# Performance work log

Hardware: AMD Instinct MI355X
Metric: run time of the kernel (lower is better)

## Reference

```python
import jax, jax.numpy as jnp
import numpy as np

BASE = 10000.0

def _rope_neox(x, positions, head_dim):
    # x: [B, S, n_heads, head_dim]; positions: [B, S] int
    half = head_dim // 2
    inv_freq = 1.0 / (BASE ** (jnp.arange(0, head_dim, 2, dtype=jnp.float32) / head_dim))  # [half]
    freqs = positions.astype(jnp.float32)[..., None] * inv_freq  # [B, S, half]
    cos = jnp.cos(freqs)[:, :, None, :]  # [B, S, 1, half]
    sin = jnp.sin(freqs)[:, :, None, :]
    x1, x2 = x[..., :half], x[..., half:]
    return jnp.concatenate([x1 * cos - x2 * sin, x2 * cos + x1 * sin], axis=-1)

def setup_inputs() -> dict:
    key = jax.random.key(0)
    k1, k2, k3 = jax.random.split(key, 3)
    B, S, H = 1, 2048, 4096
    hidden_states = jax.random.normal(k1, (B, S, H), dtype=jnp.float32)
    position_ids = jnp.broadcast_to(jnp.arange(S, dtype=jnp.int32), (B, S))
    W_qkv = jax.random.normal(k2, (H, 3 * H), dtype=jnp.float32) * (H ** -0.5)
    W_o = jax.random.normal(k3, (H, H), dtype=jnp.float32) * (H ** -0.5)
    return {"hidden_states": hidden_states, "position_ids": position_ids, "W_qkv": W_qkv, "W_o": W_o}

def reference(hidden_states, position_ids, W_qkv, W_o):
    B, S, H = hidden_states.shape
    n_heads = 32
    head_dim = H // n_heads
    qkv = hidden_states @ W_qkv  # [B, S, 3H]
    q, k, v = jnp.split(qkv, 3, axis=-1)
    q = q.reshape(B, S, n_heads, head_dim)
    k = k.reshape(B, S, n_heads, head_dim)
    v = v.reshape(B, S, n_heads, head_dim)
    q = _rope_neox(q, position_ids, head_dim)
    k = _rope_neox(k, position_ids, head_dim)
    # causal SDPA (past_key_value=None -> is_causal=True)
    scale = 1.0 / jnp.sqrt(jnp.float32(head_dim))
    scores = jnp.einsum('bqhd,bkhd->bhqk', q, k) * scale  # [B, nH, S, S]
    causal = jnp.tril(jnp.ones((S, S), dtype=bool))
    scores = jnp.where(causal, scores, jnp.finfo(scores.dtype).min)
    probs = jax.nn.softmax(scores, axis=-1)
    attn = jnp.einsum('bhqk,bkhd->bqhd', probs, v).reshape(B, S, H)
    return attn @ W_o
```

## Files before the change

kernel.cpp:

```cpp
#include <hip/hip_runtime.h>
#include <hip/hip_bf16.h>
#include <math.h>

#define SEQ   2048
#define HID   4096
#define NHEAD 32
#define HD    128
#define QKVN  12288

typedef __bf16 bf16;
typedef __bf16 bf16x8 __attribute__((ext_vector_type(8)));
typedef __bf16 bf16x4 __attribute__((ext_vector_type(4)));
typedef float  f32x4  __attribute__((ext_vector_type(4)));

#define AS1 __attribute__((address_space(1)))
#define AS3 __attribute__((address_space(3)))

__device__ __forceinline__ void gload16(const void* g, void* l) {
    __builtin_amdgcn_global_load_lds((const AS1 void*)g, (AS3 void*)l, 16, 0, 0);
}

__device__ __forceinline__ unsigned short bbits(bf16 b) {
    union { bf16 b; unsigned short u; } x; x.b = b; return x.u;
}

__global__ __launch_bounds__(512) __attribute__((amdgpu_waves_per_eu(2, 2)))
void gemm256(const bf16* __restrict__ A, const bf16* __restrict__ Bt,
             bf16* __restrict__ C, int M, int N, int K, int bcol0) {
    __shared__ __attribute__((aligned(16))) char lds[131072];
    const int tid  = threadIdx.x;
    const int l    = tid & 63;
    const int wave = tid >> 6;
    const int wr   = wave >> 2;
    const int wc   = wave & 3;
    const int lh   = l >> 4;
    const int ll   = l & 15;
    const int by   = blockIdx.x & 7, bx = blockIdx.x >> 3;
    const int brow = by * 256, bcol = bcol0 + bx * 256;

    f32x4 acc[4][4][2];
    #pragma unroll
    for (int q = 0; q < 4; ++q)
        #pragma unroll
        for (int f = 0; f < 4; ++f)
            #pragma unroll
            for (int g = 0; g < 2; ++g) acc[q][f][g] = (f32x4){0.f, 0.f, 0.f, 0.f};

    const int trow = tid >> 3, tslot = tid & 7;
    const int srcs = (tslot ^ (trow & 7)) * 16;
    const size_t rowb = (size_t)K * 2;
    const char* pA[2][2]; const char* pB[2][2];
    #pragma unroll
    for (int h = 0; h < 2; ++h)
        #pragma unroll
        for (int i = 0; i < 2; ++i) {
            pA[h][i] = (const char*)A  + (size_t)(brow + h*128 + i*64 + trow) * rowb + srcs;
            pB[h][i] = (const char*)Bt + (size_t)(bcol + h*128 + i*64 + trow) * rowb + srcs;
        }

#define SA(buf, h) do { \
        gload16(pA[h][0], lds + (buf)*65536 + (h)*16384 + tid*16); \
        gload16(pA[h][1], lds + (buf)*65536 + (h)*16384 + 8192 + tid*16); \
        pA[h][0] += 128; pA[h][1] += 128; \
    } while (0)
#define SB(buf, h) do { \
        gload16(pB[h][0], lds + (buf)*65536 + 32768 + (h)*16384 + tid*16); \
        gload16(pB[h][1], lds + (buf)*65536 + 32768 + (h)*16384 + 8192 + tid*16); \
        pB[h][0] += 128; pB[h][1] += 128; \
    } while (0)

    const int sw0 = ((0 + lh) ^ (ll & 7)) << 4;
    const int sw1 = ((4 + lh) ^ (ll & 7)) << 4;

    bf16x8 af[4][2], bv0[2][2], bv1[2][2];

#define LOADA(Xb, mh) do { \
        const char* LA_ = lds + (Xb)*65536 + (mh)*16384 + (wr*64 + ll)*128; \
        _Pragma("unroll") \
        for (int f_ = 0; f_ < 4; ++f_) { \
            af[f_][0] = *(const bf16x8*)(LA_ + f_*2048 + sw0); \
            af[f_][1] = *(const bf16x8*)(LA_ + f_*2048 + sw1); \
        } \
    } while (0)
#define LOADB(Xb, nh, bvv) do { \
        const char* LB_ = lds + (Xb)*65536 + 32768 + (nh)*16384 + (wc*32 + ll)*128; \
        _Pragma("unroll") \
        for (int g_ = 0; g_ < 2; ++g_) { \
            bvv[g_][0] = *(const bf16x8*)(LB_ + g_*2048 + sw0); \
            bvv[g_][1] = *(const bf16x8*)(LB_ + g_*2048 + sw1); \
        } \
    } while (0)
#define FENCE_MMA(WAITSTR, q, bvv) do { \
        asm volatile(WAITSTR ::: "memory"); \
        __builtin_amdgcn_s_barrier(); \
        asm volatile("s_waitcnt lgkmcnt(0)" ::: "memory"); \
        __builtin_amdgcn_sched_barrier(0); \
        __builtin_amdgcn_s_setprio(1); \
        _Pragma("unroll") \
        for (int f_ = 0; f_ < 4; ++f_) \
            _Pragma("unroll") \
            for (int g_ = 0; g_ < 2; ++g_) { \
                acc[q][f_][g_] = __builtin_amdgcn_mfma_f32_16x16x32_bf16( \
                    af[f_][0], bvv[g_][0], acc[q][f_][g_], 0, 0, 0); \
                acc[q][f_][g_] = __builtin_amdgcn_mfma_f32_16x16x32_bf16( \
                    af[f_][1], bvv[g_][1], acc[q][f_][g_], 0, 0, 0); \
            } \
        __builtin_amdgcn_s_setprio(0); \
        __builtin_amdgcn_s_barrier(); \
    } while (0)

    SA(0, 0); SB(0, 0); SB(0, 1); SA(0, 1); SA(1, 0); SB(1, 0);
    asm volatile("s_waitcnt vmcnt(8)" ::: "memory");
    __builtin_amdgcn_s_barrier();

    const int NT = K >> 6;
    for (int u = 0; u < NT - 1; ++u) {
        const int X = u & 1, Y = X ^ 1;
        LOADA(X, 0); LOADB(X, 0, bv0); SB(Y, 1);
        FENCE_MMA("s_waitcnt vmcnt(8)", 0, bv0);
        LOADB(X, 1, bv1); SA(Y, 1);
        FENCE_MMA("s_waitcnt vmcnt(8)", 1, bv1);
        LOADA(X, 1);
        if (u < NT - 2) { SA(X, 0); }
        FENCE_MMA("s_waitcnt vmcnt(8)", 2, bv0);
        if (u < NT - 2) { SB(X, 0); }
        FENCE_MMA("s_waitcnt vmcnt(8)", 3, bv1);
    }
    {
        const int X = (NT - 1) & 1;
        LOADA(X, 0); LOADB(X, 0, bv0);
        FENCE_MMA("s_waitcnt vmcnt(4)", 0, bv0);
        LOADB(X, 1, bv1);
        FENCE_MMA("s_waitcnt vmcnt(2)", 1, bv1);
        LOADA(X, 1);
        FENCE_MMA("s_waitcnt vmcnt(0)", 2, bv0);
        FENCE_MMA("s_nop 0", 3, bv1);
    }
#undef FENCE_MMA
#undef LOADA
#undef LOADB
#undef SA
#undef SB

    __syncthreads();
    float* ep = (float*)lds + wave * 2304;
    const int c8 = (l & 3) * 8;
    #pragma unroll
    for (int q = 0; q < 4; ++q) {
        const int mh = q >> 1, nh = q & 1;
        #pragma unroll
        for (int f = 0; f < 4; ++f)
            #pragma unroll
            for (int g = 0; g < 2; ++g)
                #pragma unroll
                for (int j = 0; j < 4; ++j)
                    ep[(f*16 + lh*4 + j) * 36 + g*16 + ll] = acc[q][f][g][j];
        #pragma unroll
        for (int it = 0; it < 4; ++it) {
            int r2 = it * 16 + (l >> 2);
            const float* src = ep + r2 * 36 + c8;
            bf16x8 o;
            #pragma unroll
            for (int j = 0; j < 8; ++j) o[j] = (bf16)src[j];
            size_t grow = (size_t)(brow + mh*128 + wr*64 + r2);
            *(bf16x8*)(C + grow * N + bcol + nh*128 + wc*32 + c8) = o;
        }
    }
}

template<int OB>
__global__ __launch_bounds__(512, 2) void gemm2p(const bf16* __restrict__ A,
                                                 const bf16* __restrict__ Bt,
                                                 void* __restrict__ Cv,
                                                 int M, int N, int K, int bcol0) {
    __shared__ __attribute__((aligned(16))) char lds[98304];
    const int tid  = threadIdx.x;
    const int l    = tid & 63;
    const int wave = tid >> 6;
    const int wr   = wave >> 2;
    const int wc   = wave & 3;
    const int lh   = l >> 4;
    const int ll   = l & 15;

    const int by   = blockIdx.x & 7;
    const int bx   = blockIdx.x >> 3;
    const int brow = by * 256, bcol = bcol0 + bx * 128;

    f32x4 acc[2][4][2];
    #pragma unroll
    for (int m = 0; m < 2; ++m)
        #pragma unroll
        for (int f = 0; f < 4; ++f)
            #pragma unroll
            for (int g = 0; g < 2; ++g) acc[m][f][g] = (f32x4){0.f, 0.f, 0.f, 0.f};

    const int trow = tid >> 3, tslot = tid & 7;
    const int srcs = (tslot ^ (trow & 7)) * 16;
    const size_t rowb = (size_t)K * 2;
    const char* pA[2][2]; const char* pB[2];
    #pragma unroll
    for (int h = 0; h < 2; ++h)
        #pragma unroll
        for (int i = 0; i < 2; ++i)
            pA[h][i] = (const char*)A + (size_t)(brow + h*128 + i*64 + trow) * rowb + srcs;
    #pragma unroll
    for (int i = 0; i < 2; ++i)
        pB[i] = (const char*)Bt + (size_t)(bcol + i*64 + trow) * rowb + srcs;

#define SA(buf, h) do { \
        gload16(pA[h][0], lds + (buf)*32768 + (h)*16384 + tid*16); \
        gload16(pA[h][1], lds + (buf)*32768 + (h)*16384 + 8192 + tid*16); \
        pA[h][0] += 128; pA[h][1] += 128; \
    } while (0)
#define SB(buf) do { \
        gload16(pB[0], lds + 65536 + (buf)*16384 + tid*16); \
        gload16(pB[1], lds + 65536 + (buf)*16384 + 8192 + tid*16); \
        pB[0] += 128; pB[1] += 128; \
    } while (0)

    const int sw0 = ((0 + lh) ^ (ll & 7)) << 4;
    const int sw1 = ((4 + lh) ^ (ll & 7)) << 4;

#define PHASE(Xb, mh, STAGE_STMT, WAITSTR) do { \
        const char* LA_ = lds + (Xb)*32768 + (mh)*16384 + (wr*64 + ll)*128; \
        const char* LB_ = lds + 65536 + (Xb)*16384 + (wc*32 + ll)*128; \
        bf16x8 af_[4][2], bv_[2][2]; \
        _Pragma("unroll") \
        for (int f_ = 0; f_ < 4; ++f_) { \
            af_[f_][0] = *(const bf16x8*)(LA_ + f_*2048 + sw0); \
            af_[f_][1] = *(const bf16x8*)(LA_ + f_*2048 + sw1); \
        } \
        _Pragma("unroll") \
        for (int g_ = 0; g_ < 2; ++g_) { \
            bv_[g_][0] = *(const bf16x8*)(LB_ + g_*2048 + sw0); \
            bv_[g_][1] = *(const bf16x8*)(LB_ + g_*2048 + sw1); \
        } \
        STAGE_STMT; \
        asm volatile(WAITSTR ::: "memory"); \
        __builtin_amdgcn_s_barrier(); \
        asm volatile("s_waitcnt lgkmcnt(0)" ::: "memory"); \
        __builtin_amdgcn_sched_barrier(0); \
        __builtin_amdgcn_s_setprio(1); \
        _Pragma("unroll") \
        for (int f_ = 0; f_ < 4; ++f_) \
            _Pragma("unroll") \
            for (int g_ = 0; g_ < 2; ++g_) { \
                acc[mh][f_][g_] = __builtin_amdgcn_mfma_f32_16x16x32_bf16( \
                    af_[f_][0], bv_[g_][0], acc[mh][f_][g_], 0, 0, 0); \
                acc[mh][f_][g_] = __builtin_amdgcn_mfma_f32_16x16x32_bf16( \
                    af_[f_][1], bv_[g_][1], acc[mh][f_][g_], 0, 0, 0); \
            } \
        __builtin_amdgcn_s_setprio(0); \
        __builtin_amdgcn_s_barrier(); \
    } while (0)

    SA(0, 0); SB(0); SA(0, 1); SA(1, 0);
    asm volatile("s_waitcnt vmcnt(4)" ::: "memory");
    __builtin_amdgcn_s_barrier();

    const int NT = K >> 6;
    for (int u = 0; u < NT - 2; ++u) {
        const int X = u & 1, Y = X ^ 1;
        PHASE(X, 0, SB(Y), "s_waitcnt vmcnt(4)");
        PHASE(X, 1, { SA(Y, 1); SA(X, 0); }, "s_waitcnt vmcnt(4)");
    }
    {
        const int X = (NT - 2) & 1, Y = X ^ 1;
        PHASE(X, 0, SB(Y), "s_waitcnt vmcnt(4)");
        PHASE(X, 1, SA(Y, 1), "s_waitcnt vmcnt(2)");
    }
    {
        const int X = (NT - 1) & 1;
        PHASE(X, 0, ((void)0), "s_waitcnt vmcnt(0)");
        PHASE(X, 1, ((void)0), "s_nop 0");
    }
#undef PHASE
#undef SA
#undef SB

    __syncthreads();
    float* ep = (float*)lds + wave * 2304;
    const int cq = l & 3;
    #pragma unroll
    for (int mh = 0; mh < 2; ++mh) {
        #pragma unroll
        for (int f = 0; f < 4; ++f)
            #pragma unroll
            for (int g = 0; g < 2; ++g)
                #pragma unroll
                for (int j = 0; j < 4; ++j)
                    ep[(f*16 + lh*4 + j) * 36 + g*16 + ll] = acc[mh][f][g][j];
        #pragma unroll
        for (int it = 0; it < 4; ++it) {
            int r2 = it * 16 + (l >> 2);
            const float* src = ep + r2 * 36 + cq * 8;
            size_t grow = (size_t)(brow + mh*128 + wr*64 + r2);
            int gcol = bcol + wc*32 + cq*8;
            if (OB == 0) {
                float* dst = (float*)Cv + grow * N + gcol;
                *(f32x4*)dst       = *(const f32x4*)src;
                *(f32x4*)(dst + 4) = *(const f32x4*)(src + 4);
            } else {
                bf16x8 o;
                #pragma unroll
                for (int jj = 0; jj < 8; ++jj) o[jj] = (bf16)src[jj];
                *(bf16x8*)((bf16*)Cv + grow * N + gcol) = o;
            }
        }
    }
}

__global__ __launch_bounds__(256) void cast_flat(const float* __restrict__ in,
                                                 bf16* __restrict__ out, int n8) {
    int i = blockIdx.x * 256 + threadIdx.x;
    if (i >= n8) return;
    float4 a = ((const float4*)in)[2 * i];
    float4 b = ((const float4*)in)[2 * i + 1];
    bf16x8 o = {(bf16)a.x, (bf16)a.y, (bf16)a.z, (bf16)a.w,
                (bf16)b.x, (bf16)b.y, (bf16)b.z, (bf16)b.w};
    *(bf16x8*)(out + (size_t)i * 8) = o;
}

__global__ __launch_bounds__(256) void cast_transpose(const float* __restrict__ in,
                                                      bf16* __restrict__ out, int R, int C) {
    __shared__ float t[64][65];
    const int r0 = blockIdx.y * 64, c0 = blockIdx.x * 64;
    #pragma unroll
    for (int i = 0; i < 4; ++i) {
        int idx = i * 256 + threadIdx.x;
        int rr = idx >> 4, c4 = (idx & 15) * 4;
        float4 v = *(const float4*)&in[(size_t)(r0 + rr) * C + c0 + c4];
        t[rr][c4] = v.x; t[rr][c4 + 1] = v.y; t[rr][c4 + 2] = v.z; t[rr][c4 + 3] = v.w;
    }
    __syncthreads();
    #pragma unroll
    for (int i = 0; i < 2; ++i) {
        int idx = i * 256 + threadIdx.x;
        int rr = idx >> 3, c8 = (idx & 7) * 8;
        bf16x8 o;
        #pragma unroll
        for (int j = 0; j < 8; ++j) o[j] = (bf16)t[c8 + j][rr];
        *(bf16x8*)&out[(size_t)(c0 + rr) * R + r0 + c8] = o;
    }
}

__global__ __launch_bounds__(256) void rope_table(const int* __restrict__ pos_ids,
                                                  float2* __restrict__ tab) {
    int id = blockIdx.x * 256 + threadIdx.x;
    int s = id >> 6, d = id & 63;
    float pos = (float)pos_ids[s];
    float inv = expf(-9.210340371976184f * ((float)d * (1.0f / 64.0f)));
    float sn, cs;
    sincosf(pos * inv, &sn, &cs);
    tab[id] = make_float2(cs, sn);
}

__global__ __launch_bounds__(256) void rope_repack(const bf16* __restrict__ qkv,
                                                   const float2* __restrict__ tab,
                                                   bf16* __restrict__ Qb,
                                                   bf16* __restrict__ Kb) {
    int id = blockIdx.x * 256 + threadIdx.x;
    const int d4 = (id & 15) * 4;
    const int h  = (id >> 4) & (NHEAD - 1);
    const int s  = id >> 9;

    float2 tr[4];
    #pragma unroll
    for (int i = 0; i < 4; ++i) tr[i] = tab[s * 64 + d4 + i];

    const bf16* row = qkv + (size_t)s * QKVN;
    {
        bf16x4 lo = *(const bf16x4*)(row + h * HD + d4);
        bf16x4 hi = *(const bf16x4*)(row + h * HD + 64 + d4);
        bf16x4 olo, ohi;
        #pragma unroll
        for (int i = 0; i < 4; ++i) {
            float x1 = (float)lo[i], x2 = (float)hi[i];
            olo[i] = (bf16)(x1 * tr[i].x - x2 * tr[i].y);
            ohi[i] = (bf16)(x2 * tr[i].x + x1 * tr[i].y);
        }
        bf16* qo = Qb + ((size_t)h * SEQ + s) * HD;
        *(bf16x4*)(qo + d4) = olo;
        *(bf16x4*)(qo + 64 + d4) = ohi;
    }
    {
        bf16x4 lo = *(const bf16x4*)(row + HID + h * HD + d4);
        bf16x4 hi = *(const bf16x4*)(row + HID + h * HD + 64 + d4);
        bf16x4 olo, ohi;
        #pragma unroll
        for (int i = 0; i < 4; ++i) {
            float x1 = (float)lo[i], x2 = (float)hi[i];
            olo[i] = (bf16)(x1 * tr[i].x - x2 * tr[i].y);
            ohi[i] = (bf16)(x2 * tr[i].x + x1 * tr[i].y);
        }
        bf16* ko = Kb + ((size_t)h * SEQ + s) * HD;
        *(bf16x4*)(ko + d4) = olo;
        *(bf16x4*)(ko + 64 + d4) = ohi;
    }
}

__global__ __launch_bounds__(256) void v_transpose(const bf16* __restrict__ qkv,
                                                   bf16* __restrict__ Vt) {
    __shared__ bf16 t[64][130];
    const int h = blockIdx.y, s0 = blockIdx.x * 64;
    #pragma unroll
    for (int i = 0; i < 4; ++i) {
        int idx = i * 256 + threadIdx.x;
        int ss = idx >> 4, c8 = (idx & 15) * 8;
        bf16x8 v = *(const bf16x8*)&qkv[(size_t)(s0 + ss) * QKVN + 2 * HID + h * HD + c8];
        #pragma unroll
        for (int j = 0; j < 8; ++j) t[ss][c8 + j] = v[j];
    }
    __syncthreads();
    #pragma unroll
    for (int i = 0; i < 4; ++i) {
        int idx = i * 256 + threadIdx.x;
        int dd = idx >> 3, s8 = (idx & 7) * 8;
        bf16x8 o;
        #pragma unroll
        for (int j = 0; j < 8; ++j) o[j] = t[s8 + j][dd];
        *(bf16x8*)&Vt[((size_t)h * HD + dd) * SEQ + s0 + s8] = o;
    }
}

__global__ __launch_bounds__(256) void attn_mfma(const bf16* __restrict__ Qb,
                                                 const bf16* __restrict__ Kb,
                                                 const bf16* __restrict__ Vt,
                                                 bf16* __restrict__ attn) {
    __shared__ __attribute__((aligned(16))) char Ka[2][16384];
    __shared__ __attribute__((aligned(16))) char Va[2][16384];
    __shared__ __attribute__((aligned(16))) char Ps[4 * 2048];
    const int tid  = threadIdx.x, l = tid & 63, wave = tid >> 6;
    const int head = blockIdx.x;
    const int qb   = gridDim.y - 1 - blockIdx.y;
    const int q0   = qb * 64;
    const int qw   = q0 + wave * 16;
    const float scale = 0.08838834764831845f;

    bf16x8 qf[4];
    const bf16* Qg = Qb + ((size_t)head * SEQ + qw + (l & 15)) * HD;
    #pragma unroll
    for (int kc = 0; kc < 4; ++kc) qf[kc] = *(const bf16x8*)(Qg + kc * 32 + (l >> 4) * 8);

    f32x4 o[8];
    #pragma unroll
    for (int i = 0; i < 8; ++i) o[i] = (f32x4){0.f, 0.f, 0.f, 0.f};
    float mrun = -1e30f, lrun = 0.f;
    const int qrow  = qw + (l & 15);
    const int ntile = qb + 1;

    const char* Kg = (const char*)(Kb + (size_t)head * SEQ * HD);
    const char* Vg = (const char*)(Vt + (size_t)head * HD * SEQ);
    char* Pw = Ps + wave * 2048;

#define ASTAGE(b, t0) do { \
        const int kv0_ = (t0) * 64; \
        _Pragma("unroll") \
        for (int i = 0; i < 4; ++i) { \
            int c = i * 256 + tid; \
            int rk_ = c >> 4, slk_ = c & 15; \
            gload16(Kg + (size_t)(kv0_ + rk_) * 256 + ((slk_ * 16) ^ ((rk_ & 15) << 4)), \
                    Ka[b] + (size_t)(i * 256 + (tid & 192)) * 16); \
            int rv_ = c >> 3, slv_ = c & 7; \
            gload16(Vg + (size_t)rv_ * (SEQ * 2) + (size_t)kv0_ * 2 + ((slv_ * 16) ^ ((rv_ & 7) << 4)), \
                    Va[b] + (size_t)(i * 256 + (tid & 192)) * 16); \
        } \
    } while (0)

    ASTAGE(0, 0);
    asm volatile("s_waitcnt vmcnt(0)" ::: "memory");
    __builtin_amdgcn_s_barrier();

    for (int t = 0; t < ntile; ++t) {
        const int cur = t & 1;
        const int kv0 = t * 64;
        if (t + 1 < ntile) ASTAGE(cur ^ 1, t + 1);

        f32x4 st[4];
        __builtin_amdgcn_s_setprio(1);
        #pragma unroll
        for (int mf = 0; mf < 4; ++mf) {
            f32x4 s = (f32x4){0.f, 0.f, 0.f, 0.f};
            #pragma unroll
            for (int kc = 0; kc < 4; ++kc) {
                int rk = mf * 16 + (l & 15);
                bf16x8 a = *(const bf16x8*)(Ka[cur] + rk * 256 +
                              ((kc * 64 + (l >> 4) * 16) ^ ((rk & 15) << 4)));
                s = __builtin_amdgcn_mfma_f32_16x16x32_bf16(a, qf[kc], s, 0, 0, 0);
            }
            st[mf] = s;
        }
        __builtin_amdgcn_s_setprio(0);

        float pm = -1e30f;
        #pragma unroll
        for (int mf = 0; mf < 4; ++mf)
            #pragma unroll
            for (int j = 0; j < 4; ++j) {
                int kv = kv0 + mf * 16 + (l >> 4) * 4 + j;
                float v = (kv <= qrow) ? st[mf][j] * scale : -1e30f;
                st[mf][j] = v;
                pm = fmaxf(pm, v);
            }
        pm = fmaxf(pm, __shfl_xor(pm, 16));
        pm = fmaxf(pm, __shfl_xor(pm, 32));
        float mn   = fmaxf(mrun, pm);
        float corr = __expf(mrun - mn);
        float ls = 0.f;
        #pragma unroll
        for (int mf = 0; mf < 4; ++mf)
            #pragma unroll
            for (int j = 0; j < 4; ++j) {
                float p = __expf(st[mf][j] - mn);
                st[mf][j] = p;
                ls += p;
            }
        ls += __shfl_xor(ls, 16);
        ls += __shfl_xor(ls, 32);
        lrun = lrun * corr + ls;
        mrun = mn;

        f32x4 cv;
        #pragma unroll
        for (int r = 0; r < 4; ++r) cv[r] = __shfl(corr, (l >> 4) * 4 + r, 64);
        #pragma unroll
        for (int nf = 0; nf < 8; ++nf) o[nf] *= cv;

        #pragma unroll
        for (int mf = 0; mf < 4; ++mf)
            #pragma unroll
            for (int r = 0; r < 4; r += 2) {
                int kv = mf * 16 + (l >> 4) * 4 + r;
                unsigned pk = (unsigned)bbits((bf16)st[mf][r]) |
                              ((unsigned)bbits((bf16)st[mf][r + 1]) << 16);
                *(unsigned*)(Pw + (l & 15) * 128 + ((kv * 2) ^ ((l & 15 & 7) << 4))) = pk;
            }

        __builtin_amdgcn_s_setprio(1);
        #pragma unroll
        for (int kc = 0; kc < 2; ++kc) {
            bf16x8 pa = *(const bf16x8*)(Pw + (l & 15) * 128 +
                           ((kc * 64 + (l >> 4) * 16) ^ ((l & 7) << 4)));
            #pragma unroll
            for (int nf = 0; nf < 8; ++nf) {
                int dr = nf * 16 + (l & 15);
                bf16x8 vb = *(const bf16x8*)(Va[cur] + dr * 128 +
                               ((kc * 64 + (l >> 4) * 16) ^ ((dr & 7) << 4)));
                o[nf] = __builtin_amdgcn_mfma_f32_16x16x32_bf16(pa, vb, o[nf], 0, 0, 0);
            }
        }
        __builtin_amdgcn_s_setprio(0);

        asm volatile("s_waitcnt vmcnt(0) lgkmcnt(0)" ::: "memory");
        __builtin_amdgcn_s_barrier();
    }
#undef ASTAGE

    float il = 1.0f / lrun;
    f32x4 iv;
    #pragma unroll
    for (int r = 0; r < 4; ++r) iv[r] = __shfl(il, (l >> 4) * 4 + r, 64);
    #pragma unroll
    for (int nf = 0; nf < 8; ++nf)
        #pragma unroll
        for (int r = 0; r < 4; ++r) {
            int row = qw + (l >> 4) * 4 + r;
            attn[(size_t)row * HID + head * HD + nf * 16 + (l & 15)] = (bf16)(o[nf][r] * iv[r]);
        }
}

extern "C" void kernel_launch(void* const* d_in, const int* in_sizes, int n_in,
                              void* d_out, int out_size, void* d_ws, size_t ws_size,
                              hipStream_t stream) {
    const float* hidden  = (const float*)d_in[0];
    const int*   pos_ids = (const int*)d_in[1];
    const float* W_qkv   = (const float*)d_in[2];
    const float* W_o     = (const float*)d_in[3];
    float*       out     = (float*)d_out;
    char*        ws      = (char*)d_ws;

    bf16*   Wqkv_t   = (bf16*)(ws);
    bf16*   qkv_b    = (bf16*)(ws + 100663296);
    bf16*   hidden_b = (bf16*)(ws + 150994944);
    float2* tab      = (float2*)(ws + 150994944);
    bf16* Qb     = (bf16*)(ws);
    bf16* Kb     = (bf16*)(ws + 16777216);
    bf16* Vtb    = (bf16*)(ws + 33554432);
    bf16* attn_b = (bf16*)(ws + 50331648);
    bf16* Wo_t   = (bf16*)(ws + 67108864);

    cast_flat<<<SEQ * HID / 8 / 256, 256, 0, stream>>>(hidden, hidden_b, SEQ * HID / 8);
    cast_transpose<<<dim3(QKVN / 64, HID / 64), 256, 0, stream>>>(W_qkv, Wqkv_t, HID, QKVN);
    gemm256<<<(8192 / 256) * (SEQ / 256), 512, 0, stream>>>(hidden_b, Wqkv_t, qkv_b,
                                                            SEQ, QKVN, HID, 0);
    gemm2p<1><<<(4096 / 128) * (SEQ / 256), 512, 0, stream>>>(hidden_b, Wqkv_t, qkv_b,
                                                              SEQ, QKVN, HID, 8192);
    rope_table<<<SEQ * 64 / 256, 256, 0, stream>>>(pos_ids, tab);
    rope_repack<<<SEQ * NHEAD * 16 / 256, 256, 0, stream>>>(qkv_b, tab, Qb, Kb);
    v_transpose<<<dim3(SEQ / 64, NHEAD), 256, 0, stream>>>(qkv_b, Vtb);
    cast_transpose<<<dim3(HID / 64, HID / 64), 256, 0, stream>>>(W_o, Wo_t, HID, HID);
    attn_mfma<<<dim3(NHEAD, SEQ / 64), 256, 0, stream>>>(Qb, Kb, Vtb, attn_b);
    gemm2p<0><<<(HID / 128) * (SEQ / 256), 512, 0, stream>>>(attn_b, Wo_t, out,
                                                             SEQ, HID, HID, 0);
}
```

Measured before the change: 438.3 us.

## Transpose GEMM tile to 128x256 with A fragments held across N halves

Replaces the 256x128 two-phase GEMM with a 128x256 tile variant. A fragments are loaded once per K-step and reused across two N-half phases, while B is staged in larger 32KB buffers. The block index mapping and the epilogue change to match, with a wider per-wave stride for the LDS staging of outputs. This targets LDS read traffic and global load balance in the V-projection and output GEMMs, but it changes the vmcnt pipelining and register pressure under a fixed two-waves-per-EU attribute.

```diff
diff --git a/kernel.cpp b/kernel.cpp
--- a/kernel.cpp
+++ b/kernel.cpp
@@ -169,10 +169,9 @@
 }
 
 template<int OB>
-__global__ __launch_bounds__(512, 2) void gemm2p(const bf16* __restrict__ A,
-                                                 const bf16* __restrict__ Bt,
-                                                 void* __restrict__ Cv,
-                                                 int M, int N, int K, int bcol0) {
+__global__ __launch_bounds__(512) __attribute__((amdgpu_waves_per_eu(2, 2)))
+void gemm128n(const bf16* __restrict__ A, const bf16* __restrict__ Bt,
+              void* __restrict__ Cv, int M, int N, int K, int bcol0) {
     __shared__ __attribute__((aligned(16))) char lds[98304];
     const int tid  = threadIdx.x;
     const int l    = tid & 63;
@@ -181,55 +180,55 @@
     const int wc   = wave & 3;
     const int lh   = l >> 4;
     const int ll   = l & 15;
-
-    const int by   = blockIdx.x & 7;
-    const int bx   = blockIdx.x >> 3;
-    const int brow = by * 256, bcol = bcol0 + bx * 128;
-
-    f32x4 acc[2][4][2];
-    #pragma unroll
-    for (int m = 0; m < 2; ++m)
-        #pragma unroll
-        for (int f = 0; f < 4; ++f)
-            #pragma unroll
-            for (int g = 0; g < 2; ++g) acc[m][f][g] = (f32x4){0.f, 0.f, 0.f, 0.f};
+    const int brow = (blockIdx.x & 15) * 128;
+    const int bcol = bcol0 + (blockIdx.x >> 4) * 256;
+
+    f32x4 acc[4][4];
+    #pragma unroll
+    for (int f = 0; f < 4; ++f)
+        #pragma unroll
+        for (int c = 0; c < 4; ++c) acc[f][c] = (f32x4){0.f, 0.f, 0.f, 0.f};
 
     const int trow = tid >> 3, tslot = tid & 7;
     const int srcs = (tslot ^ (trow & 7)) * 16;
     const size_t rowb = (size_t)K * 2;
-    const char* pA[2][2]; const char* pB[2];
-    #pragma unroll
-    for (int h = 0; h < 2; ++h)
-        #pragma unroll
-        for (int i = 0; i < 2; ++i)
-            pA[h][i] = (const char*)A + (size_t)(brow + h*128 + i*64 + trow) * rowb + srcs;
+    const char* pA[2]; const char* pB[4];
     #pragma unroll
     for (int i = 0; i < 2; ++i)
+        pA[i] = (const char*)A + (size_t)(brow + i*64 + trow) * rowb + srcs;
+    #pragma unroll
+    for (int i = 0; i < 4; ++i)
         pB[i] = (const char*)Bt + (size_t)(bcol + i*64 + trow) * rowb + srcs;
 
-#define SA(buf, h) do { \
-        gload16(pA[h][0], lds + (buf)*32768 + (h)*16384 + tid*16); \
-        gload16(pA[h][1], lds + (buf)*32768 + (h)*16384 + 8192 + tid*16); \
-        pA[h][0] += 128; pA[h][1] += 128; \
+#define SA(buf) do { \
+        gload16(pA[0], lds + (buf)*16384 + tid*16); \
+        gload16(pA[1], lds + (buf)*16384 + 8192 + tid*16); \
+        pA[0] += 128; pA[1] += 128; \
     } while (0)
 #define SB(buf) do { \
-        gload16(pB[0], lds + 65536 + (buf)*16384 + tid*16); \
-        gload16(pB[1], lds + 65536 + (buf)*16384 + 8192 + tid*16); \
-        pB[0] += 128; pB[1] += 128; \
+        gload16(pB[0], lds + 32768 + (buf)*32768 + tid*16); \
+        gload16(pB[1], lds + 32768 + (buf)*32768 + 8192 + tid*16); \
+        gload16(pB[2], lds + 32768 + (buf)*32768 + 16384 + tid*16); \
+        gload16(pB[3], lds + 32768 + (buf)*32768 + 24576 + tid*16); \
+        pB[0] += 128; pB[1] += 128; pB[2] += 128; pB[3] += 128; \
     } while (0)
 
     const int sw0 = ((0 + lh) ^ (ll & 7)) << 4;
     const int sw1 = ((4 + lh) ^ (ll & 7)) << 4;
 
-#define PHASE(Xb, mh, STAGE_STMT, WAITSTR) do { \
-        const char* LA_ = lds + (Xb)*32768 + (mh)*16384 + (wr*64 + ll)*128; \
-        const char* LB_ = lds + 65536 + (Xb)*16384 + (wc*32 + ll)*128; \
-        bf16x8 af_[4][2], bv_[2][2]; \
+    bf16x8 af[4][2];
+
+#define LOADA(Xb) do { \
+        const char* LA_ = lds + (Xb)*16384 + (wr*64 + ll)*128; \
         _Pragma("unroll") \
         for (int f_ = 0; f_ < 4; ++f_) { \
-            af_[f_][0] = *(const bf16x8*)(LA_ + f_*2048 + sw0); \
-            af_[f_][1] = *(const bf16x8*)(LA_ + f_*2048 + sw1); \
+            af[f_][0] = *(const bf16x8*)(LA_ + f_*2048 + sw0); \
+            af[f_][1] = *(const bf16x8*)(LA_ + f_*2048 + sw1); \
         } \
+    } while (0)
+#define PHASE(Xb, nh, STAGE_STMT, WAITSTR) do { \
+        const char* LB_ = lds + 32768 + (Xb)*32768 + (wc*64 + (nh)*32 + ll)*128; \
+        bf16x8 bv_[2][2]; \
         _Pragma("unroll") \
         for (int g_ = 0; g_ < 2; ++g_) { \
             bv_[g_][0] = *(const bf16x8*)(LB_ + g_*2048 + sw0); \
@@ -245,66 +244,71 @@
         for (int f_ = 0; f_ < 4; ++f_) \
             _Pragma("unroll") \
             for (int g_ = 0; g_ < 2; ++g_) { \
-                acc[mh][f_][g_] = __builtin_amdgcn_mfma_f32_16x16x32_bf16( \
-                    af_[f_][0], bv_[g_][0], acc[mh][f_][g_], 0, 0, 0); \
-                acc[mh][f_][g_] = __builtin_amdgcn_mfma_f32_16x16x32_bf16( \
-                    af_[f_][1], bv_[g_][1], acc[mh][f_][g_], 0, 0, 0); \
+                acc[f_][(nh)*2+g_] = __builtin_amdgcn_mfma_f32_16x16x32_bf16( \
+                    af[f_][0], bv_[g_][0], acc[f_][(nh)*2+g_], 0, 0, 0); \
+                acc[f_][(nh)*2+g_] = __builtin_amdgcn_mfma_f32_16x16x32_bf16( \
+                    af[f_][1], bv_[g_][1], acc[f_][(nh)*2+g_], 0, 0, 0); \
             } \
         __builtin_amdgcn_s_setprio(0); \
         __builtin_amdgcn_s_barrier(); \
     } while (0)
 
-    SA(0, 0); SB(0); SA(0, 1); SA(1, 0);
-    asm volatile("s_waitcnt vmcnt(4)" ::: "memory");
+    SA(0); SB(0); SA(1);
+    asm volatile("s_waitcnt vmcnt(2)" ::: "memory");
     __builtin_amdgcn_s_barrier();
 
     const int NT = K >> 6;
     for (int u = 0; u < NT - 2; ++u) {
         const int X = u & 1, Y = X ^ 1;
-        PHASE(X, 0, SB(Y), "s_waitcnt vmcnt(4)");
-        PHASE(X, 1, { SA(Y, 1); SA(X, 0); }, "s_waitcnt vmcnt(4)");
+        LOADA(X);
+        PHASE(X, 0, SB(Y), "s_waitcnt vmcnt(6)");
+        PHASE(X, 1, SA(X), "s_waitcnt vmcnt(6)");
     }
     {
         const int X = (NT - 2) & 1, Y = X ^ 1;
-        PHASE(X, 0, SB(Y), "s_waitcnt vmcnt(4)");
-        PHASE(X, 1, SA(Y, 1), "s_waitcnt vmcnt(2)");
+        LOADA(X);
+        PHASE(X, 0, SB(Y), "s_waitcnt vmcnt(6)");
+        PHASE(X, 1, ((void)0), "s_waitcnt vmcnt(4)");
     }
     {
         const int X = (NT - 1) & 1;
+        LOADA(X);
         PHASE(X, 0, ((void)0), "s_waitcnt vmcnt(0)");
         PHASE(X, 1, ((void)0), "s_nop 0");
     }
 #undef PHASE
+#undef LOADA
 #undef SA
 #undef SB
 
     __syncthreads();
-    float* ep = (float*)lds + wave * 2304;
-    const int cq = l & 3;
-    #pragma unroll
-    for (int mh = 0; mh < 2; ++mh) {
-        #pragma unroll
-        for (int f = 0; f < 4; ++f)
-            #pragma unroll
-            for (int g = 0; g < 2; ++g)
-                #pragma unroll
-                for (int j = 0; j < 4; ++j)
-                    ep[(f*16 + lh*4 + j) * 36 + g*16 + ll] = acc[mh][f][g][j];
-        #pragma unroll
-        for (int it = 0; it < 4; ++it) {
-            int r2 = it * 16 + (l >> 2);
-            const float* src = ep + r2 * 36 + cq * 8;
-            size_t grow = (size_t)(brow + mh*128 + wr*64 + r2);
-            int gcol = bcol + wc*32 + cq*8;
-            if (OB == 0) {
-                float* dst = (float*)Cv + grow * N + gcol;
-                *(f32x4*)dst       = *(const f32x4*)src;
-                *(f32x4*)(dst + 4) = *(const f32x4*)(src + 4);
-            } else {
+    float* ep = (float*)lds + wave * (16 * 68);
+    #pragma unroll
+    for (int f = 0; f < 4; ++f) {
+        #pragma unroll
+        for (int c = 0; c < 4; ++c)
+            #pragma unroll
+            for (int j = 0; j < 4; ++j)
+                ep[(lh*4 + j) * 68 + c*16 + ll] = acc[f][c][j];
+        if (OB == 0) {
+            #pragma unroll
+            for (int it = 0; it < 4; ++it) {
+                int row = it * 4 + (l >> 4);
+                const float* src = ep + row * 68 + (l & 15) * 4;
+                size_t grow = (size_t)(brow + wr*64 + f*16 + row);
+                *(f32x4*)((float*)Cv + grow * N + bcol + wc*64 + (l & 15) * 4) =
+                    *(const f32x4*)src;
+            }
+        } else {
+            #pragma unroll
+            for (int it = 0; it < 2; ++it) {
+                int row = it * 8 + (l >> 3);
+                const float* src = ep + row * 68 + (l & 7) * 8;
                 bf16x8 o;
                 #pragma unroll
-                for (int jj = 0; jj < 8; ++jj) o[jj] = (bf16)src[jj];
-                *(bf16x8*)((bf16*)Cv + grow * N + gcol) = o;
+                for (int j = 0; j < 8; ++j) o[j] = (bf16)src[j];
+                size_t grow = (size_t)(brow + wr*64 + f*16 + row);
+                *(bf16x8*)((bf16*)Cv + grow * N + bcol + wc*64 + (l & 7) * 8) = o;
             }
         }
     }
@@ -593,13 +597,13 @@
     cast_transpose<<<dim3(QKVN / 64, HID / 64), 256, 0, stream>>>(W_qkv, Wqkv_t, HID, QKVN);
     gemm256<<<(8192 / 256) * (SEQ / 256), 512, 0, stream>>>(hidden_b, Wqkv_t, qkv_b,
                                                             SEQ, QKVN, HID, 0);
-    gemm2p<1><<<(4096 / 128) * (SEQ / 256), 512, 0, stream>>>(hidden_b, Wqkv_t, qkv_b,
-                                                              SEQ, QKVN, HID, 8192);
+    gemm128n<1><<<(SEQ / 128) * (4096 / 256), 512, 0, stream>>>(hidden_b, Wqkv_t, qkv_b,
+                                                                SEQ, QKVN, HID, 8192);
     rope_table<<<SEQ * 64 / 256, 256, 0, stream>>>(pos_ids, tab);
     rope_repack<<<SEQ * NHEAD * 16 / 256, 256, 0, stream>>>(qkv_b, tab, Qb, Kb);
     v_transpose<<<dim3(SEQ / 64, NHEAD), 256, 0, stream>>>(qkv_b, Vtb);
     cast_transpose<<<dim3(HID / 64, HID / 64), 256, 0, stream>>>(W_o, Wo_t, HID, HID);
     attn_mfma<<<dim3(NHEAD, SEQ / 64), 256, 0, stream>>>(Qb, Kb, Vtb, attn_b);
-    gemm2p<0><<<(HID / 128) * (SEQ / 256), 512, 0, stream>>>(attn_b, Wo_t, out,
-                                                             SEQ, HID, HID, 0);
-}
+    gemm128n<0><<<(SEQ / 128) * (HID / 256), 512, 0, stream>>>(attn_b, Wo_t, out,
+                                                               SEQ, HID, HID, 0);
+}
```

Measured after the change: 424.5 us. 3.1% less time.
